# Kernel optimization log

Hardware: AMD Instinct MI355X
Metric: run time of the kernel (lower is better)

Reference implementation:

```python
import jax, jax.numpy as jnp
import numpy as np

B, F, E = 16384, 50, 64          # batch, field_size, embedding_size
V, D = 100000, 512               # feature_size, deep_init_size
H1, H2 = 1024, 512               # deep_layers
BN_EPS = 1e-10


def setup_inputs() -> dict:
    key = jax.random.key(0)
    ks = jax.random.split(key, 14)
    g0 = np.sqrt(6.0 / (D + H1))
    g1 = np.sqrt(6.0 / (H1 + H2))
    go = np.sqrt(5.0 / (D + 1))
    return {
        "feat_index": jax.random.randint(ks[0], (B, F), 0, V),
        "feat_value": jax.random.uniform(ks[1], (B, F), dtype=jnp.float32),
        "feature_embeddings": jax.random.normal(ks[2], (V, E), dtype=jnp.float32) * 0.01,
        "product_linear": jax.random.normal(ks[3], (D, F, E), dtype=jnp.float32) * 0.01,
        "product_bias": jax.random.normal(ks[4], (D,), dtype=jnp.float32),
        "product_quadratic_inner": jax.random.normal(ks[5], (D, F), dtype=jnp.float32) * 0.01,
        "layer_0": jax.random.uniform(ks[6], (D, H1), minval=-g0, maxval=g0, dtype=jnp.float32),
        "bias_0": jax.random.uniform(ks[7], (1, H1), minval=-g0, maxval=g0, dtype=jnp.float32),
        "layer_1": jax.random.uniform(ks[8], (H1, H2), minval=-g1, maxval=g1, dtype=jnp.float32),
        "bias_1": jax.random.uniform(ks[9], (1, H2), minval=-g1, maxval=g1, dtype=jnp.float32),
        "bn_scale": jax.random.normal(ks[10], (1,), dtype=jnp.float32) * 0.01,
        "bn_offset": jax.random.normal(ks[11], (1,), dtype=jnp.float32) * 0.01,
        "output_w": jax.random.uniform(ks[12], (H2, 1), minval=-go, maxval=go, dtype=jnp.float32),
        "output_b": jnp.float32(0.01),
    }


def reference(feat_index, feat_value, feature_embeddings, product_linear,
              product_bias, product_quadratic_inner, layer_0, bias_0,
              layer_1, bias_1, bn_scale, bn_offset, output_w, output_b):
    # embedding lookup scaled by feature values: (B, F, E)
    emb = feature_embeddings[feat_index] * feat_value[..., None]
    # linear product signal: sum over field+embed dims for each of D units
    lz = jnp.einsum('bfe,dfe->bd', emb, product_linear)          # (B, D)
    # inner quadratic signal: field-weighted sum then L2 norm over embed dim
    s = jnp.einsum('bfe,df->bde', emb, product_quadratic_inner)  # (B, D, E)
    lp = jnp.sqrt(jnp.sum(s * s, axis=-1))                       # (B, D)
    y = jax.nn.relu(lz + lp + product_bias)
    # dropout omitted (deterministic eval-mode reference)
    for W, bvec in ((layer_0, bias_0), (layer_1, bias_1)):
        y = y @ W + bvec
        m = jnp.mean(y, axis=0)
        v = jnp.var(y, axis=0)
        y = (y - m) * jax.lax.rsqrt(v + BN_EPS) * bn_scale + bn_offset
        y = jax.nn.relu(y)
    out = y @ output_w + output_b
    return jax.nn.sigmoid(out)
```

## Files before the change

### kernel.cpp

```cpp
#include <hip/hip_runtime.h>

typedef unsigned short u16;
typedef __attribute__((ext_vector_type(8))) short bf16x8v;
typedef __attribute__((ext_vector_type(4))) float f32x4v;

#define B_SZ 16384
#define F_SZ 50
#define E_SZ 64
#define D_SZ 512
#define H1_SZ 1024
#define H2_SZ 512
#define KL 3200
#define KG 1280

__device__ __forceinline__ float b2f(u16 u){
  union { unsigned int i; float f; } v; v.i = ((unsigned int)u) << 16; return v.f;
}
__device__ __forceinline__ u16 f2b(float f){
  union { float f; unsigned int i; } v; v.f = f;
  unsigned int r = v.i + 0x7FFFu + ((v.i >> 16) & 1u);
  return (u16)(r >> 16);
}

__device__ __forceinline__ void gload16(const u16* g, u16* lds_base_uniform){
#if __has_builtin(__builtin_amdgcn_global_load_lds)
  __builtin_amdgcn_global_load_lds(
      (const __attribute__((address_space(1))) unsigned int*)g,
      (__attribute__((address_space(3))) unsigned int*)lds_base_uniform,
      16, 0, 0);
#else
  int lane = threadIdx.x & 63;
  *(uint4*)(lds_base_uniform + lane*8) = *(const uint4*)g;
#endif
}

__device__ __forceinline__ void swz(int id, int nblog2, int &x, int &y){
  int xcd = id & 7, j = id >> 3;
  x = j & ((1 << nblog2) - 1);
  y = ((j >> nblog2) << 3) | xcd;
}

__global__ __launch_bounds__(256) void k_front(
    const int* __restrict__ fidx, const float* __restrict__ fval,
    const float* __restrict__ femb, u16* __restrict__ embT,
    u16* __restrict__ Gp,
    const float* __restrict__ Wl, u16* __restrict__ WlT,
    const float* __restrict__ Pq, u16* __restrict__ pqq,
    const float* __restrict__ w0, u16* __restrict__ w0T,
    const float* __restrict__ w1, u16* __restrict__ w1T,
    const float* __restrict__ pb, const float* __restrict__ b0,
    float* __restrict__ cvec)
{
  __shared__ int   sidx[F_SZ];
  __shared__ float sfv[F_SZ];
  __shared__ __align__(16) u16 tile[64*72];
  __shared__ __align__(16) u16 gbuf[KG];
  const int r = blockIdx.x, t = threadIdx.x;
  if (r < 16384){
    const int b = r;
    const int wave = t >> 6, lane = t & 63, quad = lane >> 4, l16 = lane & 15;
    if (t < F_SZ){ sidx[t] = fidx[b*F_SZ+t]; sfv[t] = fval[b*F_SZ+t]; }
    if (t < 5) gbuf[1275+t] = 0;
    __syncthreads();
    #pragma unroll
    for (int i=0;i<4;i++){
      int k4 = (i*256+t)*4;
      if (k4 < F_SZ*E_SZ){
        int f = k4>>6, e = k4&63;
        float4 v = *(const float4*)&femb[(size_t)sidx[f]*E_SZ + e];
        float s = sfv[f];
        tile[f*72+e+0] = f2b(v.x*s);
        tile[f*72+e+1] = f2b(v.y*s);
        tile[f*72+e+2] = f2b(v.z*s);
        tile[f*72+e+3] = f2b(v.w*s);
      }
    }
    __syncthreads();
    u16* orow = embT + (size_t)b*KL;
    #pragma unroll
    for (int i=0;i<2;i++){
      int k8 = (i*256+t)*8;
      if (k8 < F_SZ*E_SZ){
        int f = k8>>6, e0 = k8&63;
        *(uint4*)&orow[k8] = *(const uint4*)&tile[f*72+e0];
      }
    }
    static const int TM[10] = {0,0,0,0,1,1,1,2,2,3};
    static const int TN[10] = {0,1,2,3,1,2,3,2,3,3};
    for (int ti = wave; ti < 10; ti += 4){
      const int tm = TM[ti], tn = TN[ti];
      f32x4v g = {0.f,0.f,0.f,0.f};
      #pragma unroll
      for (int ks=0;ks<2;ks++){
        bf16x8v af = *(const bf16x8v*)&tile[(tm*16+l16)*72 + (ks*4+quad)*8];
        bf16x8v bf = *(const bf16x8v*)&tile[(tn*16+l16)*72 + (ks*4+quad)*8];
        g = __builtin_amdgcn_mfma_f32_16x16x32_bf16(af, bf, g, 0, 0, 0);
      }
      const int gn = tn*16 + l16;
      #pragma unroll
      for (int rr=0;rr<4;rr++){
        const int gm = tm*16 + quad*4 + rr;
        if (gm < F_SZ && gn < F_SZ && gn >= gm)
          gbuf[gm*F_SZ - ((gm*(gm-1))>>1) + (gn-gm)] = f2b(g[rr]);
      }
    }
    __syncthreads();
    if (t < 160)
      *(uint4*)&Gp[(size_t)b*KG + t*8] = *(const uint4*)&gbuf[t*8];
  } else if (r < 16896){
    const int d = r - 16384;
    #pragma unroll
    for (int i=0;i<4;i++){
      int k4 = (i*256+t)*4;
      if (k4 < KL){
        float4 v = *(const float4*)&Wl[(size_t)d*KL + k4];
        u16* o = &WlT[(size_t)d*KL + k4];
        o[0]=f2b(v.x); o[1]=f2b(v.y); o[2]=f2b(v.z); o[3]=f2b(v.w);
      }
    }
  } else if (r < 17408){
    const int d = r - 16896;
    const float* prow = &Pq[d*F_SZ];
    u16* orow = &pqq[(size_t)d*KG];
    int trif = 0;
    for (int f=0; f<F_SZ; f++){
      int len = F_SZ - f;
      if (t < len)
        orow[trif + t] = f2b(prow[f]*prow[f+t]*(t ? 2.f : 1.f));
      trif += len;
    }
    if (t < 5) orow[1275+t] = 0;
  } else if (r < 19456){
    int idx = (r-17408)*256 + t;
    int k = idx & 511, n = idx >> 9;
    w0T[idx] = f2b(w0[(size_t)k*H1_SZ + n]);
  } else if (r < 21504){
    int idx = (r-19456)*256 + t;
    int k = idx & 1023, n = idx >> 10;
    w1T[idx] = f2b(w1[(size_t)k*H2_SZ + n]);
  } else {
    int rr = r - 21504;
    int h = (rr & 3)*256 + t;
    int d0 = (rr >> 2)*64;
    float acc = (d0 == 0) ? b0[h] : 0.f;
    #pragma unroll 8
    for (int d=0; d<64; d++) acc += pb[d0+d]*w0[(size_t)(d0+d)*H1_SZ + h];
    atomicAdd(&cvec[h], acc);
  }
}


__global__ __launch_bounds__(256, 2) void k_prod(
    const u16* __restrict__ Ae,
    const u16* __restrict__ Bw,
    const u16* __restrict__ Ag,
    const u16* __restrict__ Bq,
    const float* __restrict__ pbias,
    u16* __restrict__ y0)
{
  __shared__ __align__(16) u16 As[128*128];
  __shared__ __align__(16) u16 Bs[128*128];
  const int tid  = threadIdx.x;
  const int wave = tid >> 6, lane = tid & 63;
  const int quad = lane >> 4, l16 = lane & 15;
  int bx, by;  swz(blockIdx.x, 2, bx, by);
  const int n0 = bx * 128, m0 = by * 128;
  const int lr4 = lane >> 4;
  const int cb  = lane & 15;
  const int sw  = (l16 & 7);

  f32x4v acc1[2][8], acc2[2][8];
  #pragma unroll
  for (int i=0;i<2;i++)
    #pragma unroll
    for (int j=0;j<8;j++){
      acc1[i][j] = (f32x4v){0.f,0.f,0.f,0.f};
      acc2[i][j] = (f32x4v){0.f,0.f,0.f,0.f};
    }

  auto run = [&](const u16* Ap, const u16* Bp, int K, f32x4v (&acc)[2][8]){
    for (int k0 = 0; k0 < K; k0 += 128){
      __syncthreads();
      #pragma unroll
      for (int c=0;c<8;c++){
        const int r0 = wave*32 + c*4;
        const int row = r0 + lr4;
        gload16(Ap + (size_t)(m0 + row)*K + k0 + ((cb ^ (row & 7)) << 3), As + r0*128);
      }
      #pragma unroll
      for (int c=0;c<8;c++){
        const int r0 = wave*32 + c*4;
        const int row = r0 + lr4;
        gload16(Bp + (size_t)(n0 + row)*K + k0 + ((cb ^ (row & 7)) << 3), Bs + r0*128);
      }
      __syncthreads();
      #pragma unroll
      for (int ks=0; ks<4; ks++){
        bf16x8v af[2], bfr[8];
        #pragma unroll
        for (int mt=0;mt<2;mt++)
          af[mt] = *(const bf16x8v*)&As[(wave*32+mt*16+l16)*128 + (((ks*4+quad) ^ sw))*8];
        #pragma unroll
        for (int nt=0;nt<8;nt++)
          bfr[nt] = *(const bf16x8v*)&Bs[(nt*16+l16)*128 + (((ks*4+quad) ^ sw))*8];
        #pragma unroll
        for (int mt=0;mt<2;mt++)
          #pragma unroll
          for (int nt=0;nt<8;nt++)
            acc[mt][nt] = __builtin_amdgcn_mfma_f32_16x16x32_bf16(af[mt], bfr[nt], acc[mt][nt], 0, 0, 0);
      }
    }
  };

  run(Ae, Bw, KL, acc1);
  run(Ag, Bq, KG, acc2);

  #pragma unroll
  for (int nt=0;nt<8;nt++){
    const int n = n0 + nt*16 + l16;
    const float bv = pbias[n];
    #pragma unroll
    for (int mt=0;mt<2;mt++){
      const int mb = m0 + wave*32 + mt*16 + quad*4;
      #pragma unroll
      for (int r=0;r<4;r++){
        float v = acc1[mt][nt][r] + sqrtf(fmaxf(acc2[mt][nt][r], 0.f)) + bv;
        v = (v > 0.f ? v : 0.f) - bv;
        y0[(size_t)(mb+r)*D_SZ + n] = f2b(v);
      }
    }
  }
}

template<int DO_STATS, int CENTER, typename CT>
__global__ __launch_bounds__(256) void gemm_bt(
    const u16* __restrict__ A, const u16* __restrict__ Bm,
    CT* __restrict__ C, const float* __restrict__ bias,
    float* __restrict__ S1, float* __restrict__ S2,
    int nblog2, int N, int K)
{
  __shared__ __align__(16) u16 As[64*128];
  __shared__ __align__(16) u16 Bs[128*128];
  const int tid  = threadIdx.x;
  const int wave = tid >> 6, lane = tid & 63;
  const int quad = lane >> 4, l16 = lane & 15;
  int bx, by;  swz(blockIdx.x, nblog2, bx, by);
  const int n0 = bx * 128, m0 = by * 64;
  const int wr = wave >> 1, wc = wave & 1;
  const int lr4 = lane >> 4;
  const int cb  = lane & 15;
  const int sw  = (l16 & 7);

  f32x4v acc[2][4];
  #pragma unroll
  for (int i=0;i<2;i++)
    #pragma unroll
    for (int j=0;j<4;j++)
      acc[i][j] = (f32x4v){0.f,0.f,0.f,0.f};

  for (int k0 = 0; k0 < K; k0 += 128){
    __syncthreads();
    #pragma unroll
    for (int c=0;c<4;c++){
      const int r0 = wave*16 + c*4;
      const int row = r0 + lr4;
      gload16(A + (size_t)(m0 + row)*K + k0 + ((cb ^ (row & 7)) << 3), As + r0*128);
    }
    #pragma unroll
    for (int c=0;c<8;c++){
      const int r0 = wave*32 + c*4;
      const int row = r0 + lr4;
      gload16(Bm + (size_t)(n0 + row)*K + k0 + ((cb ^ (row & 7)) << 3), Bs + r0*128);
    }
    __syncthreads();
    #pragma unroll
    for (int ks=0; ks<4; ks++){
      bf16x8v af[2], bfr[4];
      #pragma unroll
      for (int mt=0;mt<2;mt++)
        af[mt] = *(const bf16x8v*)&As[(wr*32+mt*16+l16)*128 + (((ks*4+quad) ^ sw))*8];
      #pragma unroll
      for (int nt=0;nt<4;nt++)
        bfr[nt] = *(const bf16x8v*)&Bs[(wc*64+nt*16+l16)*128 + (((ks*4+quad) ^ sw))*8];
      #pragma unroll
      for (int mt=0;mt<2;mt++)
        #pragma unroll
        for (int nt=0;nt<4;nt++)
          acc[mt][nt] = __builtin_amdgcn_mfma_f32_16x16x32_bf16(af[mt], bfr[nt], acc[mt][nt], 0, 0, 0);
    }
  }

  #pragma unroll
  for (int nt=0;nt<4;nt++){
    const int n = n0 + wc*64 + nt*16 + l16;
    float bv = 0.f;
    if (DO_STATS) bv = bias[n];
    float ls1 = 0.f, ls2 = 0.f;
    #pragma unroll
    for (int mt=0;mt<2;mt++){
      const int mb = m0 + wr*32 + mt*16 + quad*4;
      #pragma unroll
      for (int r=0;r<4;r++){
        float v = acc[mt][nt][r] + bv;
        if constexpr (sizeof(CT) == 2) C[(size_t)(mb+r)*N + n] = f2b(CENTER ? acc[mt][nt][r] : v);
        else                           C[(size_t)(mb+r)*N + n] = v;
        ls1 += v; ls2 += v*v;
      }
    }
    if (DO_STATS){
      ls1 += __shfl_xor(ls1, 16); ls2 += __shfl_xor(ls2, 16);
      ls1 += __shfl_xor(ls1, 32); ls2 += __shfl_xor(ls2, 32);
      if (quad == 0){ atomicAdd(&S1[n], ls1); atomicAdd(&S2[n], ls2); }
    }
  }
}

__global__ __launch_bounds__(256) void gemm_bn(
    const u16* __restrict__ Z,
    const u16* __restrict__ Bm,
    const float* __restrict__ Aa, const float* __restrict__ Bb,
    u16* __restrict__ C,
    const float* __restrict__ bias,
    float* __restrict__ S1, float* __restrict__ S2)
{
  __shared__ __align__(16) u16 As[64*128];
  __shared__ __align__(16) u16 Bs[128*128];
  const int tid  = threadIdx.x;
  const int wave = tid >> 6, lane = tid & 63;
  const int quad = lane >> 4, l16 = lane & 15;
  int bx, by;  swz(blockIdx.x, 2, bx, by);
  const int n0 = bx * 128, m0 = by * 64;
  const int wr = wave >> 1, wc = wave & 1;
  const int lr4 = lane >> 4;
  const int cb  = lane & 15;
  const int sw  = (l16 & 7);

  f32x4v acc[2][4];
  #pragma unroll
  for (int i=0;i<2;i++)
    #pragma unroll
    for (int j=0;j<4;j++)
      acc[i][j] = (f32x4v){0.f,0.f,0.f,0.f};

  for (int k0 = 0; k0 < H1_SZ; k0 += 128){
    __syncthreads();
    #pragma unroll
    for (int c=0;c<4;c++){
      const int r0 = wave*16 + c*4;
      const int row = r0 + lr4;
      const int col = k0 + ((cb ^ (row & 7)) << 3);
      union { uint4 q; u16 s[8]; } z, o;
      z.q = *(const uint4*)&Z[(size_t)(m0 + row)*H1_SZ + col];
      float4 a0 = *(const float4*)&Aa[col];
      float4 a1 = *(const float4*)&Aa[col+4];
      float4 b0 = *(const float4*)&Bb[col];
      float4 b1 = *(const float4*)&Bb[col+4];
      float av[8] = {a0.x,a0.y,a0.z,a0.w,a1.x,a1.y,a1.z,a1.w};
      float bv[8] = {b0.x,b0.y,b0.z,b0.w,b1.x,b1.y,b1.z,b1.w};
      #pragma unroll
      for (int j=0;j<8;j++){
        float v = b2f(z.s[j]) * av[j] + bv[j];
        o.s[j] = f2b(v > 0.f ? v : 0.f);
      }
      *(uint4*)&As[row*128 + cb*8] = o.q;
    }
    #pragma unroll
    for (int c=0;c<8;c++){
      const int r0 = wave*32 + c*4;
      const int row = r0 + lr4;
      gload16(Bm + (size_t)(n0 + row)*H1_SZ + k0 + ((cb ^ (row & 7)) << 3), Bs + r0*128);
    }
    __syncthreads();
    #pragma unroll
    for (int ks=0; ks<4; ks++){
      bf16x8v af[2], bfr[4];
      #pragma unroll
      for (int mt=0;mt<2;mt++)
        af[mt] = *(const bf16x8v*)&As[(wr*32+mt*16+l16)*128 + (((ks*4+quad) ^ sw))*8];
      #pragma unroll
      for (int nt=0;nt<4;nt++)
        bfr[nt] = *(const bf16x8v*)&Bs[(wc*64+nt*16+l16)*128 + (((ks*4+quad) ^ sw))*8];
      #pragma unroll
      for (int mt=0;mt<2;mt++)
        #pragma unroll
        for (int nt=0;nt<4;nt++)
          acc[mt][nt] = __builtin_amdgcn_mfma_f32_16x16x32_bf16(af[mt], bfr[nt], acc[mt][nt], 0, 0, 0);
    }
  }

  #pragma unroll
  for (int nt=0;nt<4;nt++){
    const int n = n0 + wc*64 + nt*16 + l16;
    const float bv = bias[n];
    float ls1 = 0.f, ls2 = 0.f;
    #pragma unroll
    for (int mt=0;mt<2;mt++){
      const int mb = m0 + wr*32 + mt*16 + quad*4;
      #pragma unroll
      for (int r=0;r<4;r++){
        float v = acc[mt][nt][r] + bv;
        C[(size_t)(mb+r)*H2_SZ + n] = f2b(acc[mt][nt][r]);
        ls1 += v; ls2 += v*v;
      }
    }
    ls1 += __shfl_xor(ls1, 16); ls2 += __shfl_xor(ls2, 16);
    ls1 += __shfl_xor(ls1, 32); ls2 += __shfl_xor(ls2, 32);
    if (quad == 0){ atomicAdd(&S1[n], ls1); atomicAdd(&S2[n], ls2); }
  }
}

__global__ void k_bnfin(const float* __restrict__ S1, const float* __restrict__ S2,
                        const float* __restrict__ bnsc, const float* __restrict__ bnof,
                        const float* __restrict__ cadd,
                        float* __restrict__ Aout, float* __restrict__ Bout)
{
  int i = blockIdx.x*256 + threadIdx.x;
  const float invB = 1.f / 16384.f;
  float m   = S1[i]*invB;
  float var = S2[i]*invB - m*m;
  float a   = bnsc[0] * rsqrtf(var + 1e-10f);
  Aout[i] = a;
  Bout[i] = bnof[0] - m*a + a*cadd[i];
}

__global__ __launch_bounds__(256) void k_out(
    const u16* __restrict__ Z2, const float* __restrict__ wvec,
    const float* __restrict__ obp,
    const float* __restrict__ S1, const float* __restrict__ S2,
    const float* __restrict__ bnsc, const float* __restrict__ bnof,
    const float* __restrict__ cadd,
    float* __restrict__ out)
{
  const int wave = threadIdx.x >> 6, lane = threadIdx.x & 63;
  const int b = blockIdx.x*4 + wave;
  const int n0 = lane*8;
  const float invB = 1.f / 16384.f;
  const float sc = bnsc[0], of = bnof[0];
  union { uint4 q; u16 s[8]; } z;
  z.q = *(const uint4*)&Z2[(size_t)b*H2_SZ + n0];
  float4 wa = *(const float4*)&wvec[n0];
  float4 wb = *(const float4*)&wvec[n0+4];
  float wv[8] = {wa.x,wa.y,wa.z,wa.w,wb.x,wb.y,wb.z,wb.w};
  float s = 0.f;
  #pragma unroll
  for (int j=0;j<8;j++){
    int n = n0 + j;
    float m   = S1[n]*invB;
    float var = S2[n]*invB - m*m;
    float a   = sc * rsqrtf(var + 1e-10f);
    float bb  = of - m*a + a*cadd[n];
    float y = b2f(z.s[j]) * a + bb;
    y = y > 0.f ? y : 0.f;
    s += y * wv[j];
  }
  s += __shfl_xor(s,1);  s += __shfl_xor(s,2);  s += __shfl_xor(s,4);
  s += __shfl_xor(s,8);  s += __shfl_xor(s,16); s += __shfl_xor(s,32);
  if (lane == 0){
    float x = s + obp[0];
    out[b] = 1.f / (1.f + expf(-x));
  }
}


extern "C" void kernel_launch(void* const* d_in, const int* in_sizes, int n_in,
                              void* d_out, int out_size, void* d_ws, size_t ws_size,
                              hipStream_t stream)
{
  const int*   fidx  = (const int*)d_in[0];
  const float* fval  = (const float*)d_in[1];
  const float* femb  = (const float*)d_in[2];
  const float* wl    = (const float*)d_in[3];
  const float* pbias = (const float*)d_in[4];
  const float* pq    = (const float*)d_in[5];
  const float* w0    = (const float*)d_in[6];
  const float* b0    = (const float*)d_in[7];
  const float* w1    = (const float*)d_in[8];
  const float* b1    = (const float*)d_in[9];
  const float* bnsc  = (const float*)d_in[10];
  const float* bnof  = (const float*)d_in[11];
  const float* ow    = (const float*)d_in[12];
  const float* ob    = (const float*)d_in[13];
  float* out = (float*)d_out;

  char* ws = (char*)d_ws;
  u16*   embT = (u16*)(ws + 0);
  u16*   z1b  = (u16*)(ws + 0);
  u16*   z2b  = (u16*)(ws + 100663296);
  u16*   gpb  = (u16*)(ws + 104857600);
  u16*   wlT  = (u16*)(ws + 146800640);
  u16*   pqqb = (u16*)(ws + 150077440);
  u16*   y0b  = (u16*)(ws + 151388160);
  u16*   w0T  = (u16*)(ws + 168165376);
  u16*   w1T  = (u16*)(ws + 169213952);
  float* S1a  = (float*)(ws + 170262528);
  float* S2a  = S1a + 1024;
  float* S1b  = S2a + 1024;
  float* S2b  = S1b + 512;
  float* cvec = S2b + 512;
  float* A0   = cvec + 1024;
  float* B0   = A0 + 1024;

  hipMemsetAsync((void*)S1a, 0, 16384, stream);

  k_front<<<21536, 256, 0, stream>>>(fidx, fval, femb, embT, gpb,
                                     wl, wlT, pq, pqqb, w0, w0T, w1, w1T,
                                     pbias, b0, cvec);

  k_prod<<<512, 256, 0, stream>>>(embT, wlT, gpb, pqqb, pbias, y0b);

  gemm_bt<1,1,u16><<<2048, 256, 0, stream>>>(y0b, w0T, z1b, cvec, S1a, S2a,
                                             3, H1_SZ, D_SZ);
  k_bnfin<<<4, 256, 0, stream>>>(S1a, S2a, bnsc, bnof, cvec, A0, B0);

  gemm_bn<<<1024, 256, 0, stream>>>(z1b, w1T, A0, B0, z2b, b1, S1b, S2b);

  k_out<<<4096, 256, 0, stream>>>(z2b, ow, ob, S1b, S2b, bnsc, bnof, b1, out);
}
```

Before: 339.0 us.

## Pack two rows per front block, write embT directly, prefetch A in gemm_bn

k_front now handles two batch rows per 256-thread block, with each half using 128 threads. It writes the scaled bf16 embeddings straight to global memory instead of first staging them in LDS and copying them out, and it runs the Gram MFMAs with two waves per row. gemm_bn now loads the next K-slice of Z into registers while the current MFMA step runs, overlapping global-load latency with compute at the cost of extra registers. gemm_bt's template is removed and the code is specialised to its single use.

```diff
diff --git a/kernel.cpp b/kernel.cpp
--- a/kernel.cpp
+++ b/kernel.cpp
@@ -51,49 +51,46 @@
     const float* __restrict__ pb, const float* __restrict__ b0,
     float* __restrict__ cvec)
 {
-  __shared__ int   sidx[F_SZ];
-  __shared__ float sfv[F_SZ];
-  __shared__ __align__(16) u16 tile[64*72];
-  __shared__ __align__(16) u16 gbuf[KG];
+  __shared__ int   sidx[2][F_SZ];
+  __shared__ float sfv[2][F_SZ];
+  __shared__ __align__(16) u16 tile[2][64*72];
+  __shared__ __align__(16) u16 gbuf[2][KG];
   const int r = blockIdx.x, t = threadIdx.x;
-  if (r < 16384){
-    const int b = r;
-    const int wave = t >> 6, lane = t & 63, quad = lane >> 4, l16 = lane & 15;
-    if (t < F_SZ){ sidx[t] = fidx[b*F_SZ+t]; sfv[t] = fval[b*F_SZ+t]; }
-    if (t < 5) gbuf[1275+t] = 0;
-    __syncthreads();
-    #pragma unroll
-    for (int i=0;i<4;i++){
-      int k4 = (i*256+t)*4;
+  if (r < 8192){
+    const int h  = t >> 7;
+    const int th = t & 127;
+    const int b  = r*2 + h;
+    if (th < F_SZ){ sidx[h][th] = fidx[b*F_SZ+th]; sfv[h][th] = fval[b*F_SZ+th]; }
+    if (th < 5) gbuf[h][1275+th] = 0;
+    __syncthreads();
+    u16* orow = embT + (size_t)b*KL;
+    #pragma unroll
+    for (int i=0;i<7;i++){
+      int k4 = (i*128+th)*4;
       if (k4 < F_SZ*E_SZ){
         int f = k4>>6, e = k4&63;
-        float4 v = *(const float4*)&femb[(size_t)sidx[f]*E_SZ + e];
-        float s = sfv[f];
-        tile[f*72+e+0] = f2b(v.x*s);
-        tile[f*72+e+1] = f2b(v.y*s);
-        tile[f*72+e+2] = f2b(v.z*s);
-        tile[f*72+e+3] = f2b(v.w*s);
-      }
-    }
-    __syncthreads();
-    u16* orow = embT + (size_t)b*KL;
-    #pragma unroll
-    for (int i=0;i<2;i++){
-      int k8 = (i*256+t)*8;
-      if (k8 < F_SZ*E_SZ){
-        int f = k8>>6, e0 = k8&63;
-        *(uint4*)&orow[k8] = *(const uint4*)&tile[f*72+e0];
-      }
-    }
+        float4 v = *(const float4*)&femb[(size_t)sidx[h][f]*E_SZ + e];
+        float s = sfv[h][f];
+        u16 q0=f2b(v.x*s), q1=f2b(v.y*s), q2=f2b(v.z*s), q3=f2b(v.w*s);
+        tile[h][f*72+e+0]=q0; tile[h][f*72+e+1]=q1;
+        tile[h][f*72+e+2]=q2; tile[h][f*72+e+3]=q3;
+        union { unsigned long long d; u16 s4[4]; } o4;
+        o4.s4[0]=q0; o4.s4[1]=q1; o4.s4[2]=q2; o4.s4[3]=q3;
+        *(unsigned long long*)&orow[k4] = o4.d;
+      }
+    }
+    __syncthreads();
+    const int wave = t >> 6, lane = t & 63, quad = lane >> 4, l16 = lane & 15;
+    const int hw = wave >> 1, lw = wave & 1;
     static const int TM[10] = {0,0,0,0,1,1,1,2,2,3};
     static const int TN[10] = {0,1,2,3,1,2,3,2,3,3};
-    for (int ti = wave; ti < 10; ti += 4){
+    for (int ti = lw; ti < 10; ti += 2){
       const int tm = TM[ti], tn = TN[ti];
       f32x4v g = {0.f,0.f,0.f,0.f};
       #pragma unroll
       for (int ks=0;ks<2;ks++){
-        bf16x8v af = *(const bf16x8v*)&tile[(tm*16+l16)*72 + (ks*4+quad)*8];
-        bf16x8v bf = *(const bf16x8v*)&tile[(tn*16+l16)*72 + (ks*4+quad)*8];
+        bf16x8v af = *(const bf16x8v*)&tile[hw][(tm*16+l16)*72 + (ks*4+quad)*8];
+        bf16x8v bf = *(const bf16x8v*)&tile[hw][(tn*16+l16)*72 + (ks*4+quad)*8];
         g = __builtin_amdgcn_mfma_f32_16x16x32_bf16(af, bf, g, 0, 0, 0);
       }
       const int gn = tn*16 + l16;
@@ -101,14 +98,17 @@
       for (int rr=0;rr<4;rr++){
         const int gm = tm*16 + quad*4 + rr;
         if (gm < F_SZ && gn < F_SZ && gn >= gm)
-          gbuf[gm*F_SZ - ((gm*(gm-1))>>1) + (gn-gm)] = f2b(g[rr]);
-      }
-    }
-    __syncthreads();
-    if (t < 160)
-      *(uint4*)&Gp[(size_t)b*KG + t*8] = *(const uint4*)&gbuf[t*8];
-  } else if (r < 16896){
-    const int d = r - 16384;
+          gbuf[hw][gm*F_SZ - ((gm*(gm-1))>>1) + (gn-gm)] = f2b(g[rr]);
+      }
+    }
+    __syncthreads();
+    if (t < 160){
+      #pragma unroll
+      for (int hh=0; hh<2; hh++)
+        *(uint4*)&Gp[(size_t)(r*2+hh)*KG + t*8] = *(const uint4*)&gbuf[hh][t*8];
+    }
+  } else if (r < 8704){
+    const int d = r - 8192;
     #pragma unroll
     for (int i=0;i<4;i++){
       int k4 = (i*256+t)*4;
@@ -118,8 +118,8 @@
         o[0]=f2b(v.x); o[1]=f2b(v.y); o[2]=f2b(v.z); o[3]=f2b(v.w);
       }
     }
-  } else if (r < 17408){
-    const int d = r - 16896;
+  } else if (r < 9216){
+    const int d = r - 8704;
     const float* prow = &Pq[d*F_SZ];
     u16* orow = &pqq[(size_t)d*KG];
     int trif = 0;
@@ -130,16 +130,16 @@
       trif += len;
     }
     if (t < 5) orow[1275+t] = 0;
-  } else if (r < 19456){
-    int idx = (r-17408)*256 + t;
+  } else if (r < 11264){
+    int idx = (r-9216)*256 + t;
     int k = idx & 511, n = idx >> 9;
     w0T[idx] = f2b(w0[(size_t)k*H1_SZ + n]);
-  } else if (r < 21504){
-    int idx = (r-19456)*256 + t;
+  } else if (r < 13312){
+    int idx = (r-11264)*256 + t;
     int k = idx & 1023, n = idx >> 10;
     w1T[idx] = f2b(w1[(size_t)k*H2_SZ + n]);
   } else {
-    int rr = r - 21504;
+    int rr = r - 13312;
     int h = (rr & 3)*256 + t;
     int d0 = (rr >> 2)*64;
     float acc = (d0 == 0) ? b0[h] : 0.f;
@@ -232,10 +232,9 @@
   }
 }
 
-template<int DO_STATS, int CENTER, typename CT>
 __global__ __launch_bounds__(256) void gemm_bt(
     const u16* __restrict__ A, const u16* __restrict__ Bm,
-    CT* __restrict__ C, const float* __restrict__ bias,
+    u16* __restrict__ C, const float* __restrict__ bias,
     float* __restrict__ S1, float* __restrict__ S2,
     int nblog2, int N, int K)
 {
@@ -293,8 +292,7 @@
   #pragma unroll
   for (int nt=0;nt<4;nt++){
     const int n = n0 + wc*64 + nt*16 + l16;
-    float bv = 0.f;
-    if (DO_STATS) bv = bias[n];
+    const float bv = bias[n];
     float ls1 = 0.f, ls2 = 0.f;
     #pragma unroll
     for (int mt=0;mt<2;mt++){
@@ -302,17 +300,28 @@
       #pragma unroll
       for (int r=0;r<4;r++){
         float v = acc[mt][nt][r] + bv;
-        if constexpr (sizeof(CT) == 2) C[(size_t)(mb+r)*N + n] = f2b(CENTER ? acc[mt][nt][r] : v);
-        else                           C[(size_t)(mb+r)*N + n] = v;
+        C[(size_t)(mb+r)*N + n] = f2b(acc[mt][nt][r]);
         ls1 += v; ls2 += v*v;
       }
     }
-    if (DO_STATS){
-      ls1 += __shfl_xor(ls1, 16); ls2 += __shfl_xor(ls2, 16);
-      ls1 += __shfl_xor(ls1, 32); ls2 += __shfl_xor(ls2, 32);
-      if (quad == 0){ atomicAdd(&S1[n], ls1); atomicAdd(&S2[n], ls2); }
-    }
-  }
+    ls1 += __shfl_xor(ls1, 16); ls2 += __shfl_xor(ls2, 16);
+    ls1 += __shfl_xor(ls1, 32); ls2 += __shfl_xor(ls2, 32);
+    if (quad == 0){ atomicAdd(&S1[n], ls1); atomicAdd(&S2[n], ls2); }
+  }
+}
+
+__global__ void k_bnfin(const float* __restrict__ S1, const float* __restrict__ S2,
+                        const float* __restrict__ bnsc, const float* __restrict__ bnof,
+                        const float* __restrict__ cadd,
+                        float* __restrict__ Aout, float* __restrict__ Bout)
+{
+  int i = blockIdx.x*256 + threadIdx.x;
+  const float invB = 1.f / 16384.f;
+  float m   = S1[i]*invB;
+  float var = S2[i]*invB - m*m;
+  float a   = bnsc[0] * rsqrtf(var + 1e-10f);
+  Aout[i] = a;
+  Bout[i] = bnof[0] - m*a + a*cadd[i];
 }
 
 __global__ __launch_bounds__(256) void gemm_bn(
@@ -342,21 +351,32 @@
     for (int j=0;j<4;j++)
       acc[i][j] = (f32x4v){0.f,0.f,0.f,0.f};
 
-  for (int k0 = 0; k0 < H1_SZ; k0 += 128){
-    __syncthreads();
+  uint4 zA[4];
+  auto loadA = [&](int k0){
     #pragma unroll
     for (int c=0;c<4;c++){
-      const int r0 = wave*16 + c*4;
-      const int row = r0 + lr4;
+      const int row = wave*16 + c*4 + lr4;
       const int col = k0 + ((cb ^ (row & 7)) << 3);
-      union { uint4 q; u16 s[8]; } z, o;
-      z.q = *(const uint4*)&Z[(size_t)(m0 + row)*H1_SZ + col];
+      zA[c] = *(const uint4*)&Z[(size_t)(m0 + row)*H1_SZ + col];
+    }
+  };
+
+  loadA(0);
+  for (int t = 0; t < 8; ++t){
+    const int k0 = t*128;
+    __syncthreads();
+    #pragma unroll
+    for (int c=0;c<4;c++){
+      const int row = wave*16 + c*4 + lr4;
+      const int col = k0 + ((cb ^ (row & 7)) << 3);
       float4 a0 = *(const float4*)&Aa[col];
       float4 a1 = *(const float4*)&Aa[col+4];
       float4 b0 = *(const float4*)&Bb[col];
       float4 b1 = *(const float4*)&Bb[col+4];
       float av[8] = {a0.x,a0.y,a0.z,a0.w,a1.x,a1.y,a1.z,a1.w};
       float bv[8] = {b0.x,b0.y,b0.z,b0.w,b1.x,b1.y,b1.z,b1.w};
+      union { uint4 q; u16 s[8]; } z, o;
+      z.q = zA[c];
       #pragma unroll
       for (int j=0;j<8;j++){
         float v = b2f(z.s[j]) * av[j] + bv[j];
@@ -371,6 +391,7 @@
       gload16(Bm + (size_t)(n0 + row)*H1_SZ + k0 + ((cb ^ (row & 7)) << 3), Bs + r0*128);
     }
     __syncthreads();
+    if (t < 7) loadA(k0 + 128);
     #pragma unroll
     for (int ks=0; ks<4; ks++){
       bf16x8v af[2], bfr[4];
@@ -407,20 +428,6 @@
     ls1 += __shfl_xor(ls1, 32); ls2 += __shfl_xor(ls2, 32);
     if (quad == 0){ atomicAdd(&S1[n], ls1); atomicAdd(&S2[n], ls2); }
   }
-}
-
-__global__ void k_bnfin(const float* __restrict__ S1, const float* __restrict__ S2,
-                        const float* __restrict__ bnsc, const float* __restrict__ bnof,
-                        const float* __restrict__ cadd,
-                        float* __restrict__ Aout, float* __restrict__ Bout)
-{
-  int i = blockIdx.x*256 + threadIdx.x;
-  const float invB = 1.f / 16384.f;
-  float m   = S1[i]*invB;
-  float var = S2[i]*invB - m*m;
-  float a   = bnsc[0] * rsqrtf(var + 1e-10f);
-  Aout[i] = a;
-  Bout[i] = bnof[0] - m*a + a*cadd[i];
 }
 
 __global__ __launch_bounds__(256) void k_out(
@@ -502,14 +509,14 @@
 
   hipMemsetAsync((void*)S1a, 0, 16384, stream);
 
-  k_front<<<21536, 256, 0, stream>>>(fidx, fval, femb, embT, gpb,
+  k_front<<<13344, 256, 0, stream>>>(fidx, fval, femb, embT, gpb,
                                      wl, wlT, pq, pqqb, w0, w0T, w1, w1T,
                                      pbias, b0, cvec);
 
   k_prod<<<512, 256, 0, stream>>>(embT, wlT, gpb, pqqb, pbias, y0b);
 
-  gemm_bt<1,1,u16><<<2048, 256, 0, stream>>>(y0b, w0T, z1b, cvec, S1a, S2a,
-                                             3, H1_SZ, D_SZ);
+  gemm_bt<<<2048, 256, 0, stream>>>(y0b, w0T, z1b, cvec, S1a, S2a,
+                                    3, H1_SZ, D_SZ);
   k_bnfin<<<4, 256, 0, stream>>>(S1a, S2a, bnsc, bnof, cvec, A0, B0);
 
   gemm_bn<<<1024, 256, 0, stream>>>(z1b, w1T, A0, B0, z2b, b1, S1b, S2b);
```

Result: faster. 318.1 us, median of 2 (-6.2%).
